# Kernel tuning notes

Hardware: AMD Instinct MI355X
Metric: run time of the kernel (lower is better)

Reference implementation:

```python
import jax, jax.numpy as jnp
import numpy as np

N = 50_000          # nodes
E = 1_600_000       # edges (avg degree 32)
IN = 128            # in_feats
H = 4               # num_heads
F = 32              # out_feats per head
CUTOFF = 4.0        # bessel_cutoff
P = 7               # envelope_exponent + 1
ENV_A = -(P + 1) * (P + 2) / 2.0   # -36
ENV_B = P * (P + 2)                # 63
ENV_C = -P * (P + 1) / 2.0         # -28


def setup_inputs() -> dict:
    key = jax.random.key(0)
    ks = jax.random.split(key, 8)
    x = jax.random.normal(ks[0], (N, IN), dtype=jnp.float32)
    distance = jax.random.uniform(ks[1], (E,), dtype=jnp.float32) * CUTOFF
    W_src = jax.random.normal(ks[2], (H * F, IN), dtype=jnp.float32) * 0.05
    b_src = jnp.zeros((H * F,), dtype=jnp.float32)
    W_dst = jax.random.normal(ks[3], (H * F, IN), dtype=jnp.float32) * 0.05
    b_dst = jnp.zeros((H * F,), dtype=jnp.float32)
    attn = jax.random.normal(ks[4], (1, H, F), dtype=jnp.float32) * 0.1
    prelu_alpha = jnp.full((H,), 0.25, dtype=jnp.float32)
    frequencies = jnp.arange(1.0, H + 1.0, dtype=jnp.float32) * np.pi
    src = jax.random.randint(ks[5], (E,), 0, N, dtype=jnp.int32)
    dst = jax.random.randint(ks[6], (E,), 0, N, dtype=jnp.int32)
    return dict(x=x, distance=distance, W_src=W_src, b_src=b_src,
                W_dst=W_dst, b_dst=b_dst, attn=attn,
                prelu_alpha=prelu_alpha, frequencies=frequencies,
                src=src, dst=dst)


def _bessel_coeff(distance, frequencies):
    # distance: [E] -> d_scaled: [E,1]; frequencies: [H] -> coeff: [E,H]
    d = (distance / CUTOFF)[:, None]
    d_p0 = d ** P
    env = d + ENV_A * d_p0 + ENV_B * (d_p0 * d) + ENV_C * (d_p0 * d * d)
    return env * jnp.sin(frequencies * d)


def reference(x, distance, W_src, b_src, W_dst, b_dst, attn,
              prelu_alpha, frequencies, src, dst):
    n = x.shape[0]
    feat_src = (x @ W_src.T + b_src).reshape(n, H, F)   # [N,H,F]
    feat_dst = (x @ W_dst.T + b_dst).reshape(n, H, F)   # [N,H,F]

    coeff = _bessel_coeff(distance, frequencies)[:, :, None]  # [E,H,1]

    el = feat_src[src]                                  # [E,H,F] gather
    e = (el + feat_dst[dst]) * coeff                    # u_add_v then bessel scale
    e = jnp.where(e >= 0, e, prelu_alpha[None, :, None] * e)  # PReLU per head
    score = jnp.einsum('ehf,hf->eh', e, attn[0])        # [E,H]

    # edge softmax over incoming edges per dst node, per head
    seg_max = jax.ops.segment_max(score, dst, num_segments=n)        # [N,H]
    ex = jnp.exp(score - seg_max[dst])                               # [E,H]
    denom = jax.ops.segment_sum(ex, dst, num_segments=n)             # [N,H]
    a = ex / denom[dst]                                              # [E,H]

    # u_mul_e + scatter-sum aggregation
    msgs = el * a[:, :, None]                                        # [E,H,F]
    rst = jax.ops.segment_sum(msgs, dst, num_segments=n)             # [N,H,F]
    return rst
```

## Files before the change

kernel.cpp:

```cpp
#include <hip/hip_runtime.h>
#include <hip/hip_bf16.h>
#include <math.h>

#define N_NODES 50000
#define E_EDGES 1600000
#define HF 128
#define INV_CUTOFF 0.25f
#define ENV_A -36.0f
#define ENV_B 63.0f
#define ENV_C -28.0f

#define GEMM_BLOCKS ((N_NODES + 63) / 64)
#define REC_CAP 72
#define NBUCK 196
#define BUCK_CAP 8960
#define EPB 6250
#define SPLIT 4
#define LCAP 32

typedef __attribute__((ext_vector_type(8))) short bf16x8;
typedef __attribute__((ext_vector_type(4))) float f32x4;

__device__ __forceinline__ unsigned short f2bf(float f) {
  unsigned u = __float_as_uint(f);
  u += 0x7fffu + ((u >> 16) & 1u);
  return (unsigned short)(u >> 16);
}
__device__ __forceinline__ unsigned pack2(float lo, float hi) {
  return (unsigned)f2bf(lo) | ((unsigned)f2bf(hi) << 16);
}
__device__ __forceinline__ float2 up2(unsigned v) {
  return make_float2(__uint_as_float(v << 16), __uint_as_float(v & 0xffff0000u));
}

__device__ __forceinline__ float2 pk_add(float2 a, float2 b) {
  float2 d;
  asm("v_pk_add_f32 %0, %1, %2" : "=v"(d) : "v"(a), "v"(b));
  return d;
}
__device__ __forceinline__ float2 pk_fma(float2 a, float2 b, float2 c) {
  float2 d;
  asm("v_pk_fma_f32 %0, %1, %2, %3" : "=v"(d) : "v"(a), "v"(b), "v"(c));
  return d;
}
__device__ __forceinline__ float2 pk_abs(float2 a) {
  float2 d;
  d.x = __uint_as_float(__float_as_uint(a.x) & 0x7fffffffu);
  d.y = __uint_as_float(__float_as_uint(a.y) & 0x7fffffffu);
  return d;
}

__global__ void prep_w(const float* __restrict__ Ws, const float* __restrict__ Wd,
                       unsigned short* __restrict__ wbf) {
  const int q = blockIdx.x * 256 + threadIdx.x;
  if (q < 4096) {
    const int n = q >> 4, c = q & 15;
    const float* Wp = ((n < 128) ? Ws : Wd) + (size_t)(n & 127) * HF + c * 8;
    const float4 v0 = *(const float4*)Wp;
    const float4 v1 = *(const float4*)(Wp + 4);
    uint4 pk;
    pk.x = pack2(v0.x, v0.y); pk.y = pack2(v0.z, v0.w);
    pk.z = pack2(v1.x, v1.y); pk.w = pack2(v1.z, v1.w);
    *(uint4*)(wbf + (size_t)n * HF + ((c ^ (n & 15)) * 8)) = pk;
  }
}

__global__ __launch_bounds__(256) void feat_gemm(
    const float* __restrict__ x, const unsigned short* __restrict__ wbf,
    const float* __restrict__ bs, const float* __restrict__ bd,
    unsigned short* __restrict__ fs, float* __restrict__ fd) {
  __shared__ unsigned short wlds[256 * 128];

  for (int i = threadIdx.x; i < 4096; i += 256)
    ((uint4*)wlds)[i] = ((const uint4*)wbf)[i];

  const int lane = threadIdx.x & 63;
  const int wave = threadIdx.x >> 6;
  const int m = lane & 15;
  const int quad = lane >> 4;
  const int m0 = blockIdx.x * 64 + wave * 16;
  const int row = m0 + m;
  const int rowc = (row < N_NODES) ? row : (N_NODES - 1);

  union { bf16x8 v; unsigned u[4]; } af[4];
  #pragma unroll
  for (int kt = 0; kt < 4; kt++) {
    const float* xp = x + (size_t)rowc * HF + kt * 32 + quad * 8;
    const float4 u0 = *(const float4*)xp;
    const float4 u1 = *(const float4*)(xp + 4);
    af[kt].u[0] = pack2(u0.x, u0.y); af[kt].u[1] = pack2(u0.z, u0.w);
    af[kt].u[2] = pack2(u1.x, u1.y); af[kt].u[3] = pack2(u1.z, u1.w);
  }

  __syncthreads();

  float accA[16][4];
  #pragma unroll
  for (int nt = 0; nt < 16; nt++) {
    const int nrow = nt * 16 + m;
    f32x4 acc = {0.f, 0.f, 0.f, 0.f};
    #pragma unroll
    for (int kt = 0; kt < 4; kt++) {
      const int pc = (kt * 4 + quad) ^ m;
      const bf16x8 bf = *(const bf16x8*)(wlds + (size_t)nrow * HF + pc * 8);
      acc = __builtin_amdgcn_mfma_f32_16x16x32_bf16(af[kt].v, bf, acc, 0, 0, 0);
    }
    accA[nt][0] = acc[0]; accA[nt][1] = acc[1];
    accA[nt][2] = acc[2]; accA[nt][3] = acc[3];
  }

  __syncthreads();
  unsigned short* fsS = wlds;
  float* fdS = (float*)(wlds + 64 * 136);

  const int rl0 = wave * 16 + quad * 4;
  #pragma unroll
  for (int nt = 0; nt < 16; nt++) {
    const int col = nt * 16 + m;
    if (col < 128) {
      const float bias = bs[col];
      #pragma unroll
      for (int r = 0; r < 4; r++)
        fsS[(rl0 + r) * 136 + col] = f2bf(accA[nt][r] + bias);
    } else {
      const float bias = bd[col - 128];
      #pragma unroll
      for (int r = 0; r < 4; r++)
        fdS[(rl0 + r) * 132 + (col - 128)] = accA[nt][r] + bias;
    }
  }
  __syncthreads();

  for (int c = threadIdx.x; c < 1024; c += 256) {
    const int r = c >> 4, off = (c & 15) * 8;
    const int gr = blockIdx.x * 64 + r;
    if (gr < N_NODES)
      *(uint4*)(fs + (size_t)gr * HF + off) = *(const uint4*)(fsS + r * 136 + off);
  }
  for (int c = threadIdx.x; c < 2048; c += 256) {
    const int r = c >> 5, off = (c & 31) * 4;
    const int gr = blockIdx.x * 64 + r;
    if (gr < N_NODES)
      *(float4*)(fd + (size_t)gr * HF + off) = *(const float4*)(fdS + r * 132 + off);
  }
}

__global__ __launch_bounds__(256) void bucketize(
    const int* __restrict__ dst, const int* __restrict__ src,
    const float* __restrict__ dist,
    int* __restrict__ bcursor, unsigned* __restrict__ bb_pay,
    unsigned char* __restrict__ bb_loc) {
  __shared__ unsigned pay_s[EPB];
  __shared__ unsigned char bkt_s[EPB];
  __shared__ unsigned char loc_s[EPB];
  __shared__ int hist[NBUCK], loff[NBUCK], base[NBUCK], cur[NBUCK];
  for (int t = threadIdx.x; t < NBUCK; t += 256) { hist[t] = 0; cur[t] = 0; }
  __syncthreads();
  const int lo = blockIdx.x * EPB;
  for (int k = threadIdx.x; k < EPB; k += 256)
    atomicAdd(&hist[dst[lo + k] >> 8], 1);
  __syncthreads();
  if (threadIdx.x == 0) {
    int run = 0;
    for (int j = 0; j < NBUCK; j++) { loff[j] = run; run += hist[j]; }
  }
  __syncthreads();
  for (int t = threadIdx.x; t < NBUCK; t += 256)
    base[t] = atomicAdd(&bcursor[t], hist[t]);
  __syncthreads();
  for (int k = threadIdx.x; k < EPB; k += 256) {
    const int d = dst[lo + k];
    const int b = d >> 8;
    float ds = dist[lo + k] * (INV_CUTOFF * 65536.f);
    unsigned dq = (unsigned)(ds + 0.5f);
    if (dq > 65535u) dq = 65535u;
    const int s = loff[b] + atomicAdd(&cur[b], 1);
    pay_s[s] = (unsigned)src[lo + k] | (dq << 16);
    bkt_s[s] = (unsigned char)b;
    loc_s[s] = (unsigned char)(d & 255);
  }
  __syncthreads();
  for (int s = threadIdx.x; s < EPB; s += 256) {
    const int b = bkt_s[s];
    const int dest = base[b] + (s - loff[b]);
    if (dest < BUCK_CAP) {
      bb_pay[(size_t)b * BUCK_CAP + dest] = pay_s[s];
      bb_loc[(size_t)b * BUCK_CAP + dest] = loc_s[s];
    }
  }
}

__global__ __launch_bounds__(256) void bucket_scatter(
    const int* __restrict__ bcursor, const unsigned* __restrict__ bb_pay,
    const unsigned char* __restrict__ bb_loc,
    int* __restrict__ counts, unsigned* __restrict__ rec) {
  __shared__ int cnt[256];
  __shared__ unsigned recS[256 * LCAP];
  cnt[threadIdx.x] = 0;
  __syncthreads();
  const int b = blockIdx.x / SPLIT;
  const int q = blockIdx.x - b * SPLIT;
  const int total = min(bcursor[b], BUCK_CAP);
  const int lo = (total * q) / SPLIT;
  const int hi = (total * (q + 1)) / SPLIT;
  const size_t base = (size_t)b * BUCK_CAP;
  for (int i = lo + threadIdx.x; i < hi; i += 256) {
    const unsigned pay = bb_pay[base + i];
    const int local = bb_loc[base + i];
    const int r = atomicAdd(&cnt[local], 1);
    if (r < LCAP) recS[local * LCAP + r] = pay;
  }
  __syncthreads();
  const int node = (b << 8) + (int)threadIdx.x;
  if (node < N_NODES) {
    const int cl = min(cnt[threadIdx.x], LCAP);
    if (cl > 0) {
      const int gbase = atomicAdd(&counts[node], cl);
      unsigned* dstp = rec + (size_t)node * REC_CAP;
      const unsigned* srcp = recS + threadIdx.x * LCAP;
      for (int k = 0; k < cl; k++) {
        const int pos = gbase + k;
        if (pos < REC_CAP) dstp[pos] = srcp[k];
      }
    }
  }
}

__global__ __launch_bounds__(256) void gat_agg(
    const unsigned short* __restrict__ fs, const float* __restrict__ fd,
    const int* __restrict__ counts, const unsigned* __restrict__ rec,
    const float* __restrict__ attn, const float* __restrict__ alpha_p,
    const float* __restrict__ freqs, float* __restrict__ out) {
  const int wave = threadIdx.x >> 6;
  const int lane = threadIdx.x & 63;
  const int n = lane >> 5;
  const int e = (lane >> 3) & 3;
  const int h = (lane >> 1) & 3;
  const int j = lane & 1;
  const int fo = (h << 5) + (j << 4);

  const int node = blockIdx.x * 8 + wave * 2 + n;
  const bool vnode = (node < N_NODES);
  const int nodec = vnode ? node : (N_NODES - 1);

  int cnt = vnode ? counts[node] : 0;
  cnt = (cnt < REC_CAP) ? cnt : REC_CAP;

  const float* fdp = fd + (size_t)nodec * HF + fo;
  float2 f0 = *(const float2*)(fdp + 0),  f1 = *(const float2*)(fdp + 2);
  float2 f2 = *(const float2*)(fdp + 4),  f3 = *(const float2*)(fdp + 6);
  float2 f4 = *(const float2*)(fdp + 8),  f5 = *(const float2*)(fdp + 10);
  float2 f6 = *(const float2*)(fdp + 12), f7 = *(const float2*)(fdp + 14);
  const float* tp = attn + fo;
  float2 t0 = *(const float2*)(tp + 0),  t1 = *(const float2*)(tp + 2);
  float2 t2 = *(const float2*)(tp + 4),  t3 = *(const float2*)(tp + 6);
  float2 t4 = *(const float2*)(tp + 8),  t5 = *(const float2*)(tp + 10);
  float2 t6 = *(const float2*)(tp + 12), t7 = *(const float2*)(tp + 14);

  const float al = alpha_p[h];
  const float c1 = 0.5f * (1.0f + al);
  const float c2 = 0.5f * (1.0f - al);
  const float fr = freqs[h];

  const int beg = nodec * REC_CAP;
  const unsigned short* fsp = fs + fo;

  float l = 0.f;
  float2 A0 = {0.f,0.f}, A1 = {0.f,0.f}, A2 = {0.f,0.f}, A3 = {0.f,0.f};
  float2 A4 = {0.f,0.f}, A5 = {0.f,0.f}, A6 = {0.f,0.f}, A7 = {0.f,0.f};

  for (int idx = e; idx < cnt; idx += 4) {
    const unsigned r = rec[beg + idx];
    const unsigned short* rowp = fsp + ((size_t)(r & 0xffffu) << 7);
    const uint4 b0 = *(const uint4*)(rowp);
    const uint4 b1 = *(const uint4*)(rowp + 8);
    const float2 e0 = up2(b0.x), e1 = up2(b0.y), e2 = up2(b0.z), e3 = up2(b0.w);
    const float2 e4 = up2(b1.x), e5 = up2(b1.y), e6 = up2(b1.z), e7 = up2(b1.w);

    const float d = (float)(r >> 16) * (1.0f / 65536.0f);
    const float d2 = d * d;
    const float d4 = d2 * d2;
    const float d7 = d4 * d2 * d;
    const float env = fmaf(d7, fmaf(d, fmaf(d, ENV_C, ENV_B), ENV_A), d);
    const float cf = env * __sinf(fr * d);
    const float k1 = c1 * cf;
    const float k2 = c2 * fabsf(cf);

    float2 D1 = {0.f, 0.f}, D2 = {0.f, 0.f};
    float2 u;
    u = pk_add(e0, f0); D1 = pk_fma(u, t0, D1); D2 = pk_fma(pk_abs(u), t0, D2);
    u = pk_add(e1, f1); D1 = pk_fma(u, t1, D1); D2 = pk_fma(pk_abs(u), t1, D2);
    u = pk_add(e2, f2); D1 = pk_fma(u, t2, D1); D2 = pk_fma(pk_abs(u), t2, D2);
    u = pk_add(e3, f3); D1 = pk_fma(u, t3, D1); D2 = pk_fma(pk_abs(u), t3, D2);
    u = pk_add(e4, f4); D1 = pk_fma(u, t4, D1); D2 = pk_fma(pk_abs(u), t4, D2);
    u = pk_add(e5, f5); D1 = pk_fma(u, t5, D1); D2 = pk_fma(pk_abs(u), t5, D2);
    u = pk_add(e6, f6); D1 = pk_fma(u, t6, D1); D2 = pk_fma(pk_abs(u), t6, D2);
    u = pk_add(e7, f7); D1 = pk_fma(u, t7, D1); D2 = pk_fma(pk_abs(u), t7, D2);

    float p = fmaf(k1, D1.x + D1.y, k2 * (D2.x + D2.y));
    p += __shfl_xor(p, 1);

    const float w = __expf(p);
    l += w;
    const float2 w2 = {w, w};
    A0 = pk_fma(w2, e0, A0); A1 = pk_fma(w2, e1, A1);
    A2 = pk_fma(w2, e2, A2); A3 = pk_fma(w2, e3, A3);
    A4 = pk_fma(w2, e4, A4); A5 = pk_fma(w2, e5, A5);
    A6 = pk_fma(w2, e6, A6); A7 = pk_fma(w2, e7, A7);
  }

  #pragma unroll
  for (int mm = 8; mm <= 16; mm <<= 1) {
    l    += __shfl_xor(l, mm);
    A0.x += __shfl_xor(A0.x, mm); A0.y += __shfl_xor(A0.y, mm);
    A1.x += __shfl_xor(A1.x, mm); A1.y += __shfl_xor(A1.y, mm);
    A2.x += __shfl_xor(A2.x, mm); A2.y += __shfl_xor(A2.y, mm);
    A3.x += __shfl_xor(A3.x, mm); A3.y += __shfl_xor(A3.y, mm);
    A4.x += __shfl_xor(A4.x, mm); A4.y += __shfl_xor(A4.y, mm);
    A5.x += __shfl_xor(A5.x, mm); A5.y += __shfl_xor(A5.y, mm);
    A6.x += __shfl_xor(A6.x, mm); A6.y += __shfl_xor(A6.y, mm);
    A7.x += __shfl_xor(A7.x, mm); A7.y += __shfl_xor(A7.y, mm);
  }

  if (e == 0 && vnode) {
    const float rl = (l > 0.f) ? 1.0f / l : 0.f;
    float* o = out + (size_t)node * HF + fo;
    float4 o0 = {A0.x * rl, A0.y * rl, A1.x * rl, A1.y * rl};
    float4 o1 = {A2.x * rl, A2.y * rl, A3.x * rl, A3.y * rl};
    float4 o2 = {A4.x * rl, A4.y * rl, A5.x * rl, A5.y * rl};
    float4 o3 = {A6.x * rl, A6.y * rl, A7.x * rl, A7.y * rl};
    *(float4*)(o + 0)  = o0;
    *(float4*)(o + 4)  = o1;
    *(float4*)(o + 8)  = o2;
    *(float4*)(o + 12) = o3;
  }
}

extern "C" void kernel_launch(void* const* d_in, const int* in_sizes, int n_in,
                              void* d_out, int out_size, void* d_ws, size_t ws_size,
                              hipStream_t stream) {
  const float* x      = (const float*)d_in[0];
  const float* dist   = (const float*)d_in[1];
  const float* W_src  = (const float*)d_in[2];
  const float* b_src  = (const float*)d_in[3];
  const float* W_dst  = (const float*)d_in[4];
  const float* b_dst  = (const float*)d_in[5];
  const float* attn   = (const float*)d_in[6];
  const float* alpha  = (const float*)d_in[7];
  const float* freqs  = (const float*)d_in[8];
  const int*   src    = (const int*)d_in[9];
  const int*   dst    = (const int*)d_in[10];
  float* out = (float*)d_out;

  char* w = (char*)d_ws;
  size_t off = 0;
  auto alloc = [&](size_t bytes) -> void* {
    void* p = w + off;
    off += (bytes + 255) & ~(size_t)255;
    return p;
  };
  unsigned short* feat_src = (unsigned short*)alloc((size_t)N_NODES * HF * 2);
  float*          feat_dst = (float*)alloc((size_t)N_NODES * HF * 4);
  unsigned short* wbf      = (unsigned short*)alloc((size_t)256 * HF * 2);
  int*            counts   = (int*)alloc((size_t)N_NODES * 4);
  int*            bcursor  = (int*)alloc((size_t)NBUCK * 4);
  unsigned*       bb_pay   = (unsigned*)alloc((size_t)NBUCK * BUCK_CAP * 4);
  unsigned char*  bb_loc   = (unsigned char*)alloc((size_t)NBUCK * BUCK_CAP);
  unsigned*       rec      = (unsigned*)alloc((size_t)NBUCK * 256 * REC_CAP * 4);

  hipMemsetAsync(bcursor, 0, (size_t)NBUCK * 4, stream);
  hipMemsetAsync(counts, 0, (size_t)N_NODES * 4, stream);

  prep_w<<<16, 256, 0, stream>>>(W_src, W_dst, wbf);

  feat_gemm<<<GEMM_BLOCKS, 256, 0, stream>>>(x, wbf, b_src, b_dst, feat_src, feat_dst);

  bucketize<<<256, 256, 0, stream>>>(dst, src, dist, bcursor, bb_pay, bb_loc);

  bucket_scatter<<<NBUCK * SPLIT, 256, 0, stream>>>(bcursor, bb_pay, bb_loc, counts, rec);

  gat_agg<<<(N_NODES + 7) / 8, 256, 0, stream>>>(
      feat_src, feat_dst, counts, rec, attn, alpha, freqs, out);
}
```

Measured before the change: 248.8 us.

## Fuse memsets into prep_w, read GEMM weights from global, one node per wave

Zeroing of counts and bucket cursors moves into the weight-prep kernel, replacing two memset calls. The GEMM stops staging the full bf16 weight matrix into LDS and reads MFMA B fragments directly from global/L2 memory. The aggregation kernel assigns one node per wave with 8 edge slots in parallel, masking tail edges, instead of two nodes per wave with 4 slots. This trades LDS staging and syncs for more global traffic, and halves loop trip counts per node at the cost of more waves and wasted masked lanes.

```diff
diff --git a/kernel.cpp b/kernel.cpp
--- a/kernel.cpp
+++ b/kernel.cpp
@@ -50,8 +50,10 @@
   return d;
 }
 
-__global__ void prep_w(const float* __restrict__ Ws, const float* __restrict__ Wd,
-                       unsigned short* __restrict__ wbf) {
+__global__ __launch_bounds__(256) void prep_w(
+    const float* __restrict__ Ws, const float* __restrict__ Wd,
+    unsigned short* __restrict__ wbf, int* __restrict__ counts,
+    int* __restrict__ bcursor) {
   const int q = blockIdx.x * 256 + threadIdx.x;
   if (q < 4096) {
     const int n = q >> 4, c = q & 15;
@@ -61,18 +63,18 @@
     uint4 pk;
     pk.x = pack2(v0.x, v0.y); pk.y = pack2(v0.z, v0.w);
     pk.z = pack2(v1.x, v1.y); pk.w = pack2(v1.z, v1.w);
-    *(uint4*)(wbf + (size_t)n * HF + ((c ^ (n & 15)) * 8)) = pk;
-  }
+    *(uint4*)(wbf + (size_t)n * HF + c * 8) = pk;
+  }
+  if (q < NBUCK) bcursor[q] = 0;
+  if (q < N_NODES) counts[q] = 0;
 }
 
 __global__ __launch_bounds__(256) void feat_gemm(
     const float* __restrict__ x, const unsigned short* __restrict__ wbf,
     const float* __restrict__ bs, const float* __restrict__ bd,
     unsigned short* __restrict__ fs, float* __restrict__ fd) {
-  __shared__ unsigned short wlds[256 * 128];
-
-  for (int i = threadIdx.x; i < 4096; i += 256)
-    ((uint4*)wlds)[i] = ((const uint4*)wbf)[i];
+  __shared__ unsigned short fsS[64 * 136];
+  __shared__ float fdS[64 * 132];
 
   const int lane = threadIdx.x & 63;
   const int wave = threadIdx.x >> 6;
@@ -92,8 +94,6 @@
     af[kt].u[2] = pack2(u1.x, u1.y); af[kt].u[3] = pack2(u1.z, u1.w);
   }
 
-  __syncthreads();
-
   float accA[16][4];
   #pragma unroll
   for (int nt = 0; nt < 16; nt++) {
@@ -101,17 +101,12 @@
     f32x4 acc = {0.f, 0.f, 0.f, 0.f};
     #pragma unroll
     for (int kt = 0; kt < 4; kt++) {
-      const int pc = (kt * 4 + quad) ^ m;
-      const bf16x8 bf = *(const bf16x8*)(wlds + (size_t)nrow * HF + pc * 8);
+      const bf16x8 bf = *(const bf16x8*)(wbf + (size_t)nrow * HF + kt * 32 + quad * 8);
       acc = __builtin_amdgcn_mfma_f32_16x16x32_bf16(af[kt].v, bf, acc, 0, 0, 0);
     }
     accA[nt][0] = acc[0]; accA[nt][1] = acc[1];
     accA[nt][2] = acc[2]; accA[nt][3] = acc[3];
   }
-
-  __syncthreads();
-  unsigned short* fsS = wlds;
-  float* fdS = (float*)(wlds + 64 * 136);
 
   const int rl0 = wave * 16 + quad * 4;
   #pragma unroll
@@ -226,27 +221,21 @@
   }
 }
 
-__global__ __launch_bounds__(256) void gat_agg(
+__global__ __launch_bounds__(256, 4) void gat_agg(
     const unsigned short* __restrict__ fs, const float* __restrict__ fd,
     const int* __restrict__ counts, const unsigned* __restrict__ rec,
     const float* __restrict__ attn, const float* __restrict__ alpha_p,
     const float* __restrict__ freqs, float* __restrict__ out) {
   const int wave = threadIdx.x >> 6;
   const int lane = threadIdx.x & 63;
-  const int n = lane >> 5;
-  const int e = (lane >> 3) & 3;
+  const int node = blockIdx.x * 4 + wave;
+  if (node >= N_NODES) return;
+  const int e = lane >> 3;
   const int h = (lane >> 1) & 3;
   const int j = lane & 1;
   const int fo = (h << 5) + (j << 4);
 
-  const int node = blockIdx.x * 8 + wave * 2 + n;
-  const bool vnode = (node < N_NODES);
-  const int nodec = vnode ? node : (N_NODES - 1);
-
-  int cnt = vnode ? counts[node] : 0;
-  cnt = (cnt < REC_CAP) ? cnt : REC_CAP;
-
-  const float* fdp = fd + (size_t)nodec * HF + fo;
+  const float* fdp = fd + (size_t)node * HF + fo;
   float2 f0 = *(const float2*)(fdp + 0),  f1 = *(const float2*)(fdp + 2);
   float2 f2 = *(const float2*)(fdp + 4),  f3 = *(const float2*)(fdp + 6);
   float2 f4 = *(const float2*)(fdp + 8),  f5 = *(const float2*)(fdp + 10);
@@ -262,15 +251,21 @@
   const float c2 = 0.5f * (1.0f - al);
   const float fr = freqs[h];
 
-  const int beg = nodec * REC_CAP;
+  const int beg = node * REC_CAP;
+  int cnt = counts[node];
+  cnt = (cnt < REC_CAP) ? cnt : REC_CAP;
+  const int end = beg + cnt;
+  const int last = end - 1;
   const unsigned short* fsp = fs + fo;
 
   float l = 0.f;
   float2 A0 = {0.f,0.f}, A1 = {0.f,0.f}, A2 = {0.f,0.f}, A3 = {0.f,0.f};
   float2 A4 = {0.f,0.f}, A5 = {0.f,0.f}, A6 = {0.f,0.f}, A7 = {0.f,0.f};
 
-  for (int idx = e; idx < cnt; idx += 4) {
-    const unsigned r = rec[beg + idx];
+  for (int i = beg; i < end; i += 8) {
+    const int ii = i + e;
+    const bool valid = (ii < end);
+    const unsigned r = rec[valid ? ii : last];
     const unsigned short* rowp = fsp + ((size_t)(r & 0xffffu) << 7);
     const uint4 b0 = *(const uint4*)(rowp);
     const uint4 b1 = *(const uint4*)(rowp + 8);
@@ -300,7 +295,7 @@
     float p = fmaf(k1, D1.x + D1.y, k2 * (D2.x + D2.y));
     p += __shfl_xor(p, 1);
 
-    const float w = __expf(p);
+    const float w = valid ? __expf(p) : 0.f;
     l += w;
     const float2 w2 = {w, w};
     A0 = pk_fma(w2, e0, A0); A1 = pk_fma(w2, e1, A1);
@@ -310,7 +305,7 @@
   }
 
   #pragma unroll
-  for (int mm = 8; mm <= 16; mm <<= 1) {
+  for (int mm = 8; mm <= 32; mm <<= 1) {
     l    += __shfl_xor(l, mm);
     A0.x += __shfl_xor(A0.x, mm); A0.y += __shfl_xor(A0.y, mm);
     A1.x += __shfl_xor(A1.x, mm); A1.y += __shfl_xor(A1.y, mm);
@@ -322,7 +317,7 @@
     A7.x += __shfl_xor(A7.x, mm); A7.y += __shfl_xor(A7.y, mm);
   }
 
-  if (e == 0 && vnode) {
+  if (e == 0) {
     const float rl = (l > 0.f) ? 1.0f / l : 0.f;
     float* o = out + (size_t)node * HF + fo;
     float4 o0 = {A0.x * rl, A0.y * rl, A1.x * rl, A1.y * rl};
@@ -368,10 +363,7 @@
   unsigned char*  bb_loc   = (unsigned char*)alloc((size_t)NBUCK * BUCK_CAP);
   unsigned*       rec      = (unsigned*)alloc((size_t)NBUCK * 256 * REC_CAP * 4);
 
-  hipMemsetAsync(bcursor, 0, (size_t)NBUCK * 4, stream);
-  hipMemsetAsync(counts, 0, (size_t)N_NODES * 4, stream);
-
-  prep_w<<<16, 256, 0, stream>>>(W_src, W_dst, wbf);
+  prep_w<<<256, 256, 0, stream>>>(W_src, W_dst, wbf, counts, bcursor);
 
   feat_gemm<<<GEMM_BLOCKS, 256, 0, stream>>>(x, wbf, b_src, b_dst, feat_src, feat_dst);
 
@@ -379,6 +371,6 @@
 
   bucket_scatter<<<NBUCK * SPLIT, 256, 0, stream>>>(bcursor, bb_pay, bb_loc, counts, rec);
 
-  gat_agg<<<(N_NODES + 7) / 8, 256, 0, stream>>>(
+  gat_agg<<<(N_NODES + 3) / 4, 256, 0, stream>>>(
       feat_src, feat_dst, counts, rec, attn, alpha, freqs, out);
 }
```

Result: slower. 271.2 us (+9.0%).
